# Performance work log

Measured on AMD Instinct MI355X. Metric: run time of the kernel, lower is better.

Reference implementation:

```python
import jax, jax.numpy as jnp
import numpy as np

FLOW_ITERS = 8
DUAL_ITERS = 8
DUAL_STEP = 0.1
DUAL_MOM = 0.9
GRAPH_LAYERS = 2
BIG = 1e9


def _sparsemax(z, mask):
    # sparsemax along last axis; masked entries already hold -BIG, zeroed by mask after.
    V = z.shape[-1]
    zs = jnp.sort(z, axis=-1)[..., ::-1]
    cum = jnp.cumsum(zs, axis=-1)
    k = jnp.arange(1, V + 1, dtype=z.dtype)
    support = zs * k > (cum - 1.0)
    k_sel = jnp.sum(support.astype(jnp.int32), axis=-1, keepdims=True)
    tau = (jnp.take_along_axis(cum, k_sel - 1, axis=-1) - 1.0) / k_sel.astype(z.dtype)
    return jnp.maximum(z - tau, 0.0) * mask


def _min_cost_flow(props, demands):
    # iterative proportional flow routing: push relu(inflow - demand) along predicted proportions
    def body(flow, _):
        inflow = jnp.sum(flow, axis=1)[..., None]      # [B,V,1] inflow to each node
        adjusted = jax.nn.relu(inflow - demands)       # excess to re-route
        return props * adjusted, None                  # row i scaled by its excess
    flow0 = jnp.zeros_like(props)
    flow, _ = jax.lax.scan(body, flow0, None, length=FLOW_ITERS)
    return flow


def _dual_flow(dual_diff, adj):
    # Nesterov-momentum projected gradient on cost(x)=x^2 minus linear dual term, x>=0 on edges
    def body(carry, _):
        flow, acc = carry
        look = flow - DUAL_MOM * acc
        grad = 2.0 * look - dual_diff                  # d/dx x^2 - dual_diff
        acc = DUAL_MOM * acc + DUAL_STEP * grad
        flow = adj * jax.nn.relu(flow - acc)
        return (flow, acc), None
    z = jnp.zeros_like(dual_diff)
    (flow, _), _ = jax.lax.scan(body, (z, z), None, length=DUAL_ITERS)
    return flow


def setup_inputs():
    key = jax.random.key(0)
    ks = jax.random.split(key, 32)
    B, V, F, E, D, K, H = 8, 1200, 8, 16, 64, 2, 4
    node_features = jax.random.normal(ks[0], (B, V, F), dtype=jnp.float32)
    node_embeddings = jax.random.normal(ks[1], (B, V, E), dtype=jnp.float32)
    d = jax.random.normal(ks[2], (B, V, 1), dtype=jnp.float32)
    demands = d - jnp.mean(d, axis=1, keepdims=True)   # balanced supply/demand per graph
    eye = jnp.eye(V, dtype=jnp.float32)
    adj = (jax.random.uniform(ks[3], (B, V, V)) < (16.0 / V)).astype(jnp.float32) * (1.0 - eye)
    hop2 = jnp.clip(adj @ adj, 0.0, 1.0) * (1.0 - eye)
    neighborhoods = jnp.stack([adj, hop2], axis=0)     # [K,B,V,V] k-hop neighborhoods

    def dense(k, fin, fout):
        return (jax.random.normal(k, (fin, fout), dtype=jnp.float32) / np.sqrt(fin)).astype(jnp.float32)

    return dict(
        node_features=node_features, node_embeddings=node_embeddings,
        demands=demands, adj=adj, neighborhoods=neighborhoods,
        enc_w0=dense(ks[4], E + F, D), enc_b0=jnp.zeros((D,), jnp.float32),
        enc_w1=dense(ks[5], D, D), enc_b1=jnp.zeros((D,), jnp.float32),
        agg_w=(jax.random.normal(ks[6], (K, D, D)) / np.sqrt(D)).astype(jnp.float32),
        agg_b=jnp.zeros((K, D), jnp.float32),
        att_w=(jax.random.normal(ks[7], (H, D, D)) / np.sqrt(D)).astype(jnp.float32),
        att_b=jnp.zeros((H, D), jnp.float32),
        att_v=(jax.random.normal(ks[8], (H, D)) / np.sqrt(D)).astype(jnp.float32),
        gru_wu=dense(ks[9], 2 * D, D), gru_bu=jnp.zeros((D,), jnp.float32),
        gru_wr=dense(ks[10], 2 * D, D), gru_br=jnp.zeros((D,), jnp.float32),
        gru_wc=dense(ks[11], 2 * D, D), gru_bc=jnp.zeros((D,), jnp.float32),
        dec_w0=dense(ks[12], D, D), dec_b0=jnp.zeros((D,), jnp.float32),
        dec_w1=dense(ks[13], D, 1), dec_b1=jnp.zeros((1,), jnp.float32),
        dual_w0=dense(ks[14], D, D), dual_b0=jnp.zeros((D,), jnp.float32),
        dual_w1=dense(ks[15], D, 1), dual_b1=jnp.zeros((1,), jnp.float32),
    )


def reference(node_features, node_embeddings, demands, adj, neighborhoods,
              enc_w0, enc_b0, enc_w1, enc_b1, agg_w, agg_b, att_w, att_b, att_v,
              gru_wu, gru_bu, gru_wr, gru_br, gru_wc, gru_bc,
              dec_w0, dec_b0, dec_w1, dec_b1, dual_w0, dual_b0, dual_w1, dual_b1):
    H = att_w.shape[0]
    # node encoder MLP (tanh hidden, tanh final since activate_final=True)
    x = jnp.concatenate([node_embeddings, node_features], axis=-1)
    enc = jnp.tanh(jnp.tanh(x @ enc_w0 + enc_b0) @ enc_w1 + enc_b1)            # [B,V,D]

    deg = jnp.sum(neighborhoods, axis=-1, keepdims=True)
    nb_norm = neighborhoods / jnp.maximum(deg, 1.0)                            # [K,B,V,V]

    for _ in range(GRAPH_LAYERS):
        # per-hop neighborhood aggregation
        msg = jnp.einsum('kbuv,bvd->kbud', nb_norm, enc)
        agg = jnp.tanh(jnp.einsum('kbud,kde->kbue', msg, agg_w) + agg_b[:, None, None, :])
        # multi-head attention over the K hop levels
        proj = jnp.tanh(jnp.einsum('kbvd,hde->hkbve', agg, att_w) + att_b[:, None, None, None, :])
        scores = jnp.einsum('hkbve,he->hkbv', proj, att_v)
        attn = jax.nn.softmax(scores, axis=1)                                  # softmax over hops
        nxt = jnp.einsum('hkbv,kbvd->bvd', attn, agg) / H                      # mean over heads
        # GRU state update
        xs = jnp.concatenate([nxt, enc], axis=-1)
        u = jax.nn.sigmoid(xs @ gru_wu + gru_bu)
        r = jax.nn.sigmoid(xs @ gru_wr + gru_br)
        c = jnp.tanh(jnp.concatenate([nxt, r * enc], axis=-1) @ gru_wc + gru_bc)
        enc = u * enc + (1.0 - u) * c

    # primal: edge weights -> sparsemax -> min-cost-flow
    pred = (enc @ dec_w0 + dec_b0) @ dec_w1 + dec_b1                           # [B,V,1]
    pred_weights = adj * jnp.transpose(pred, (0, 2, 1))                        # [B,V,V]
    weights = -BIG * (1.0 - adj) + pred_weights
    flow_props = _sparsemax(weights, adj)
    flow = _min_cost_flow(flow_props, demands)
    flow_cost = jnp.sum(flow * flow, axis=(1, 2))                              # square cost

    # dual: potentials -> dual-diff -> dual flow solver
    dual = (enc @ dual_w0 + dual_b0) @ dual_w1 + dual_b1                       # [B,V,1]
    dual_diff = adj * (dual - jnp.transpose(dual, (0, 2, 1)))
    dflow = _dual_flow(dual_diff, adj)
    dual_demand = jnp.sum(dual * demands, axis=(1, 2))
    dual_cost = jnp.sum(dflow * dflow - dual_diff * dflow, axis=(1, 2)) - dual_demand

    return flow_cost - dual_cost                                               # duality-gap loss, [B]
```

## Files before the change

### kernel.cpp

```cpp
#include <hip/hip_runtime.h>

#define BB 8
#define VV 1200
#define DD 64
#define KH 2
#define NH 4
#define CAP 64
#define NB2CAP 384
#define NROW (BB*VV)
#define NKROW (KH*BB*VV)

__device__ __forceinline__ float wredsum(float v) {
#pragma unroll
  for (int o = 32; o > 0; o >>= 1) v += __shfl_xor(v, o, 64);
  return v;
}
__device__ __forceinline__ float gredsum32(float v) {
#pragma unroll
  for (int o = 16; o > 0; o >>= 1) v += __shfl_xor(v, o, 64);
  return v;
}

__device__ __forceinline__ float tanh_f(float x) {
  float e = __expf(2.0f * x);
  return 1.0f - 2.0f / (e + 1.0f);
}
__device__ __forceinline__ float sigmoid_f(float x) { return 1.0f / (1.0f + __expf(-x)); }

__device__ __forceinline__ unsigned pack_bf16x2(float a, float b) {
  unsigned ua = __float_as_uint(a), ub = __float_as_uint(b);
  ua = (ua + 0x7fffu + ((ua >> 16) & 1u)) >> 16;
  ub = (ub + 0x7fffu + ((ub >> 16) & 1u)) & 0xffff0000u;
  return ua | ub;
}
__device__ __forceinline__ float bf_lo(unsigned u) { return __uint_as_float(u << 16); }
__device__ __forceinline__ float bf_hi(unsigned u) { return __uint_as_float(u & 0xffff0000u); }

__device__ __forceinline__ size_t nb_base(int row) {
  return (row < NROW) ? (size_t)row * CAP
                      : (size_t)NROW * CAP + (size_t)(row - NROW) * NB2CAP;
}

#define ENC2B (NROW / 64)
#define CSR2B (NKROW / 8)
__global__ void __launch_bounds__(512) k_pre(
    const float* __restrict__ nb, int* __restrict__ nb_cols, int* __restrict__ nb_cnt,
    const float* __restrict__ emb, const float* __restrict__ feat,
    const float* __restrict__ w0, const float* __restrict__ b0,
    const float* __restrict__ w1, const float* __restrict__ b1,
    unsigned* __restrict__ enc0,
    int* __restrict__ col_cnt, float* __restrict__ out, int out_size) {
  __shared__ float Xe[64][25];
  __shared__ float Ht[64][65];
  int bid = blockIdx.x;
  int tid = threadIdx.x;
  if (bid < ENC2B) {
    int tile0 = bid * 64;
    if (tid < 256) {
      int i = tid >> 2, f = tid & 3;
      float4 e4 = *(const float4*)(emb + (size_t)(tile0 + i) * 16 + f * 4);
      Xe[i][f * 4] = e4.x; Xe[i][f * 4 + 1] = e4.y; Xe[i][f * 4 + 2] = e4.z; Xe[i][f * 4 + 3] = e4.w;
    } else if (tid < 384) {
      int t = tid - 256; int i = t >> 1, f = t & 1;
      float4 f4 = *(const float4*)(feat + (size_t)(tile0 + i) * 8 + f * 4);
      Xe[i][16 + f * 4] = f4.x; Xe[i][16 + f * 4 + 1] = f4.y;
      Xe[i][16 + f * 4 + 2] = f4.z; Xe[i][16 + f * 4 + 3] = f4.w;
    }
    __syncthreads();
    int rsub = tid >> 4, cg = tid & 15;
    int c0 = cg * 4, r0 = rsub * 2;
    float a[2][4];
#pragma unroll
    for (int i = 0; i < 2; ++i)
#pragma unroll
      for (int j = 0; j < 4; ++j) a[i][j] = b0[c0 + j];
#pragma unroll
    for (int kk = 0; kk < 24; ++kk) {
      float4 w4 = *(const float4*)(w0 + kk * DD + c0);
      float x0 = Xe[r0][kk], x1 = Xe[r0 + 1][kk];
      a[0][0] = fmaf(x0, w4.x, a[0][0]); a[0][1] = fmaf(x0, w4.y, a[0][1]);
      a[0][2] = fmaf(x0, w4.z, a[0][2]); a[0][3] = fmaf(x0, w4.w, a[0][3]);
      a[1][0] = fmaf(x1, w4.x, a[1][0]); a[1][1] = fmaf(x1, w4.y, a[1][1]);
      a[1][2] = fmaf(x1, w4.z, a[1][2]); a[1][3] = fmaf(x1, w4.w, a[1][3]);
    }
#pragma unroll
    for (int i = 0; i < 2; ++i) {
      Ht[r0 + i][c0] = tanh_f(a[i][0]); Ht[r0 + i][c0 + 1] = tanh_f(a[i][1]);
      Ht[r0 + i][c0 + 2] = tanh_f(a[i][2]); Ht[r0 + i][c0 + 3] = tanh_f(a[i][3]);
    }
    __syncthreads();
    float g[2][4];
#pragma unroll
    for (int i = 0; i < 2; ++i)
#pragma unroll
      for (int j = 0; j < 4; ++j) g[i][j] = b1[c0 + j];
#pragma unroll 8
    for (int kk = 0; kk < DD; ++kk) {
      float4 w4 = *(const float4*)(w1 + kk * DD + c0);
      float x0 = Ht[r0][kk], x1 = Ht[r0 + 1][kk];
      g[0][0] = fmaf(x0, w4.x, g[0][0]); g[0][1] = fmaf(x0, w4.y, g[0][1]);
      g[0][2] = fmaf(x0, w4.z, g[0][2]); g[0][3] = fmaf(x0, w4.w, g[0][3]);
      g[1][0] = fmaf(x1, w4.x, g[1][0]); g[1][1] = fmaf(x1, w4.y, g[1][1]);
      g[1][2] = fmaf(x1, w4.z, g[1][2]); g[1][3] = fmaf(x1, w4.w, g[1][3]);
    }
#pragma unroll
    for (int i = 0; i < 2; ++i) {
      uint2 pk;
      pk.x = pack_bf16x2(tanh_f(g[i][0]), tanh_f(g[i][1]));
      pk.y = pack_bf16x2(tanh_f(g[i][2]), tanh_f(g[i][3]));
      ((uint2*)enc0)[(size_t)(tile0 + r0 + i) * 16 + cg] = pk;
    }
  } else if (bid < ENC2B + CSR2B) {
    int w = tid >> 6, lane = tid & 63;
    int row = (bid - ENC2B) * 8 + w;
    const float4* nb4 = (const float4*)(nb + (size_t)row * VV);
    float4 v[5];
#pragma unroll
    for (int c = 0; c < 4; ++c) v[c] = nb4[c * 64 + lane];
    v[4].x = v[4].y = v[4].z = v[4].w = 0.0f;
    if (lane < 44) v[4] = nb4[256 + lane];
    unsigned long long ltmask = (lane == 0) ? 0ull : ((1ull << lane) - 1ull);
    size_t base = nb_base(row);
    int cap = (row < NROW) ? CAP : NB2CAP;
    int off_base = 0;
#pragma unroll
    for (int c = 0; c < 5; ++c) {
      int nz0 = (v[c].x != 0.0f), nz1 = (v[c].y != 0.0f);
      int nz2 = (v[c].z != 0.0f), nz3 = (v[c].w != 0.0f);
      unsigned long long m0 = __ballot(nz0 != 0);
      unsigned long long m1 = __ballot(nz1 != 0);
      unsigned long long m2 = __ballot(nz2 != 0);
      unsigned long long m3 = __ballot(nz3 != 0);
      int lanepref = __popcll(m0 & ltmask) + __popcll(m1 & ltmask)
                   + __popcll(m2 & ltmask) + __popcll(m3 & ltmask);
      int chunkcnt = __popcll(m0) + __popcll(m1) + __popcll(m2) + __popcll(m3);
      int off = off_base + lanepref;
      int vi = (c * 64 + lane) * 4;
      if (nz0 && off < cap) nb_cols[base + off] = vi;
      off += nz0;
      if (nz1 && off < cap) nb_cols[base + off] = vi + 1;
      off += nz1;
      if (nz2 && off < cap) nb_cols[base + off] = vi + 2;
      off += nz2;
      if (nz3 && off < cap) nb_cols[base + off] = vi + 3;
      off_base += chunkcnt;
    }
    if (lane == 0) nb_cnt[row] = (off_base > cap) ? cap : off_base;
  } else {
    for (int i = tid; i < NROW; i += 512) col_cnt[i] = 0;
    if (tid < out_size) out[tid] = 0.0f;
  }
}

__global__ void __launch_bounds__(256) k_gather(
    const int* __restrict__ nb_cols, const int* __restrict__ nb_cnt,
    const unsigned* __restrict__ encIn, float* __restrict__ msg) {
  int w = threadIdx.x >> 6, lane = threadIdx.x & 63;
  int row = blockIdx.x * 4 + w;
  int k = (row >= NROW) ? 1 : 0;
  int bv = row - k * NROW;
  int b = bv / VV;
  const uint2* encU = (const uint2*)(encIn + (size_t)b * VV * 32);
  const int* cols = nb_cols + nb_base(row);
  int n = nb_cnt[row];
  int sub = lane >> 4, q = lane & 15;
  float ax = 0.0f, ay = 0.0f, az = 0.0f, aw = 0.0f;
  int j = 0;
  int cc0 = 0, cc1 = 0, cc2 = 0, cc3 = 0;
  if (j + 16 <= n) {
    cc0 = cols[j + sub]; cc1 = cols[j + 4 + sub];
    cc2 = cols[j + 8 + sub]; cc3 = cols[j + 12 + sub];
  }
  while (j + 16 <= n) {
    int nj = j + 16;
    int p0 = 0, p1 = 0, p2 = 0, p3 = 0;
    if (nj + 16 <= n) {
      p0 = cols[nj + sub]; p1 = cols[nj + 4 + sub];
      p2 = cols[nj + 8 + sub]; p3 = cols[nj + 12 + sub];
    }
    uint2 u0 = encU[(size_t)cc0 * 16 + q];
    uint2 u1 = encU[(size_t)cc1 * 16 + q];
    uint2 u2 = encU[(size_t)cc2 * 16 + q];
    uint2 u3 = encU[(size_t)cc3 * 16 + q];
    ax += (bf_lo(u0.x) + bf_lo(u1.x)) + (bf_lo(u2.x) + bf_lo(u3.x));
    ay += (bf_hi(u0.x) + bf_hi(u1.x)) + (bf_hi(u2.x) + bf_hi(u3.x));
    az += (bf_lo(u0.y) + bf_lo(u1.y)) + (bf_lo(u2.y) + bf_lo(u3.y));
    aw += (bf_hi(u0.y) + bf_hi(u1.y)) + (bf_hi(u2.y) + bf_hi(u3.y));
    cc0 = p0; cc1 = p1; cc2 = p2; cc3 = p3;
    j = nj;
  }
  for (; j < n; j += 4) {
    int idx = j + sub;
    if (idx < n) {
      uint2 u = encU[(size_t)cols[idx] * 16 + q];
      ax += bf_lo(u.x); ay += bf_hi(u.x); az += bf_lo(u.y); aw += bf_hi(u.y);
    }
  }
#pragma unroll
  for (int o = 16; o < 64; o <<= 1) {
    ax += __shfl_xor(ax, o, 64);
    ay += __shfl_xor(ay, o, 64);
    az += __shfl_xor(az, o, 64);
    aw += __shfl_xor(aw, o, 64);
  }
  if (lane < 16) {
    float inv = 1.0f / fmaxf((float)n, 1.0f);
    float4 r; r.x = ax * inv; r.y = ay * inv; r.z = az * inv; r.w = aw * inv;
    ((float4*)(msg + (size_t)row * DD))[q] = r;
  }
}

__global__ void __launch_bounds__(512) k_mlp(
    const float* __restrict__ msg,
    const float* __restrict__ agg_w, const float* __restrict__ agg_b,
    const float* __restrict__ att_w, const float* __restrict__ att_b,
    const float* __restrict__ att_v,
    float* __restrict__ agg, float* __restrict__ scores) {
  __shared__ float M[64][65];
  __shared__ float G[64][65];
  int tid = threadIdx.x;
  int tile0 = blockIdx.x * 64;
  int k = (tile0 >= NROW) ? 1 : 0;
  int bv0 = tile0 - k * NROW;
  int strip = tid >> 5, cg2 = tid & 31;
  int c0 = cg2 * 2;
  int r0 = strip * 4;
#pragma unroll
  for (int rep = 0; rep < 2; ++rep) {
    int idx = rep * 512 + tid; int i = idx >> 4, d4 = idx & 15;
    float4 m4 = *(const float4*)(msg + (size_t)(tile0 + i) * DD + d4 * 4);
    M[i][d4 * 4] = m4.x; M[i][d4 * 4 + 1] = m4.y; M[i][d4 * 4 + 2] = m4.z; M[i][d4 * 4 + 3] = m4.w;
  }
  __syncthreads();
  const float* W = agg_w + (size_t)k * DD * DD;
  float acc[4][2];
#pragma unroll
  for (int i = 0; i < 4; ++i) {
    acc[i][0] = agg_b[k * DD + c0]; acc[i][1] = agg_b[k * DD + c0 + 1];
  }
#pragma unroll 8
  for (int kk = 0; kk < DD; ++kk) {
    float2 w2 = *(const float2*)(W + kk * DD + c0);
#pragma unroll
    for (int i = 0; i < 4; ++i) {
      float x = M[r0 + i][kk];
      acc[i][0] = fmaf(x, w2.x, acc[i][0]); acc[i][1] = fmaf(x, w2.y, acc[i][1]);
    }
  }
#pragma unroll
  for (int i = 0; i < 4; ++i) {
    float g0 = tanh_f(acc[i][0]), g1 = tanh_f(acc[i][1]);
    G[r0 + i][c0] = g0; G[r0 + i][c0 + 1] = g1;
    *(float2*)(agg + (size_t)(tile0 + r0 + i) * DD + c0) = make_float2(g0, g1);
  }
  __syncthreads();
#pragma unroll
  for (int h = 0; h < NH; ++h) {
    const float* Wh = att_w + (size_t)h * DD * DD;
    float a2[4][2];
#pragma unroll
    for (int i = 0; i < 4; ++i) {
      a2[i][0] = att_b[h * DD + c0]; a2[i][1] = att_b[h * DD + c0 + 1];
    }
#pragma unroll 8
    for (int kk = 0; kk < DD; ++kk) {
      float2 w2 = *(const float2*)(Wh + kk * DD + c0);
#pragma unroll
      for (int i = 0; i < 4; ++i) {
        float x = G[r0 + i][kk];
        a2[i][0] = fmaf(x, w2.x, a2[i][0]); a2[i][1] = fmaf(x, w2.y, a2[i][1]);
      }
    }
    float2 v2 = *(const float2*)(att_v + h * DD + c0);
#pragma unroll
    for (int i = 0; i < 4; ++i) {
      float p = tanh_f(a2[i][0]) * v2.x + tanh_f(a2[i][1]) * v2.y;
      p = gredsum32(p);
      if (cg2 == 0) scores[(size_t)(h * KH + k) * NROW + bv0 + r0 + i] = p;
    }
  }
}

__global__ void __launch_bounds__(128) k_gru(
    const unsigned* __restrict__ encIn, const float* __restrict__ agg,
    const float* __restrict__ scores,
    const float* __restrict__ wu, const float* __restrict__ bu,
    const float* __restrict__ wr, const float* __restrict__ br,
    const float* __restrict__ wc, const float* __restrict__ bc,
    unsigned* __restrict__ encOut,
    int do_decode,
    const float* __restrict__ dw0, const float* __restrict__ db0,
    const float* __restrict__ dw1, const float* __restrict__ db1,
    const float* __restrict__ uw0, const float* __restrict__ ub0,
    const float* __restrict__ uw1, const float* __restrict__ ub1,
    float* __restrict__ pred, float* __restrict__ dualp) {
  __shared__ float X[16][129];
  __shared__ float EO[16][65];
  int tid = threadIdx.x;
  int tile0 = blockIdx.x * 16;
  int strip = tid >> 5, cg2 = tid & 31;
  int c0 = cg2 * 2;
  int r0 = strip * 4;
#pragma unroll
  for (int rep = 0; rep < 2; ++rep) {
    int idx = rep * 128 + tid; int i = idx >> 4, d4 = idx & 15;
    int row = tile0 + i;
    float W0 = 0.0f, W1 = 0.0f;
#pragma unroll
    for (int h = 0; h < NH; ++h) {
      float s0 = scores[(size_t)(h * KH + 0) * NROW + row];
      float s1 = scores[(size_t)(h * KH + 1) * NROW + row];
      float m = fmaxf(s0, s1);
      float e0 = __expf(s0 - m), e1 = __expf(s1 - m);
      float inv = 1.0f / (e0 + e1);
      W0 += e0 * inv; W1 += e1 * inv;
    }
    W0 *= 0.25f; W1 *= 0.25f;
    uint2 eu = ((const uint2*)encIn)[(size_t)row * 16 + d4];
    float4 a0 = *(const float4*)(agg + (size_t)row * DD + d4 * 4);
    float4 a1 = *(const float4*)(agg + (size_t)(NROW + row) * DD + d4 * 4);
    X[i][d4 * 4]     = W0 * a0.x + W1 * a1.x;
    X[i][d4 * 4 + 1] = W0 * a0.y + W1 * a1.y;
    X[i][d4 * 4 + 2] = W0 * a0.z + W1 * a1.z;
    X[i][d4 * 4 + 3] = W0 * a0.w + W1 * a1.w;
    X[i][64 + d4 * 4]     = bf_lo(eu.x);
    X[i][64 + d4 * 4 + 1] = bf_hi(eu.x);
    X[i][64 + d4 * 4 + 2] = bf_lo(eu.y);
    X[i][64 + d4 * 4 + 3] = bf_hi(eu.y);
  }
  __syncthreads();
  float au[4][2], ar[4][2];
#pragma unroll
  for (int i = 0; i < 4; ++i) {
    au[i][0] = bu[c0]; au[i][1] = bu[c0 + 1];
    ar[i][0] = br[c0]; ar[i][1] = br[c0 + 1];
  }
#pragma unroll 8
  for (int kk = 0; kk < 2 * DD; ++kk) {
    float2 u2 = *(const float2*)(wu + kk * DD + c0);
    float2 r2 = *(const float2*)(wr + kk * DD + c0);
#pragma unroll
    for (int i = 0; i < 4; ++i) {
      float x = X[r0 + i][kk];
      au[i][0] = fmaf(x, u2.x, au[i][0]); au[i][1] = fmaf(x, u2.y, au[i][1]);
      ar[i][0] = fmaf(x, r2.x, ar[i][0]); ar[i][1] = fmaf(x, r2.y, ar[i][1]);
    }
  }
  float uu[4][2], encv[4][2];
#pragma unroll
  for (int i = 0; i < 4; ++i) {
    uu[i][0] = sigmoid_f(au[i][0]); uu[i][1] = sigmoid_f(au[i][1]);
    encv[i][0] = X[r0 + i][64 + c0]; encv[i][1] = X[r0 + i][64 + c0 + 1];
  }
  __syncthreads();
#pragma unroll
  for (int i = 0; i < 4; ++i) {
    X[r0 + i][64 + c0]     = encv[i][0] * sigmoid_f(ar[i][0]);
    X[r0 + i][64 + c0 + 1] = encv[i][1] * sigmoid_f(ar[i][1]);
  }
  __syncthreads();
  float ac[4][2];
#pragma unroll
  for (int i = 0; i < 4; ++i) { ac[i][0] = bc[c0]; ac[i][1] = bc[c0 + 1]; }
#pragma unroll 8
  for (int kk = 0; kk < 2 * DD; ++kk) {
    float2 c2 = *(const float2*)(wc + kk * DD + c0);
#pragma unroll
    for (int i = 0; i < 4; ++i) {
      float x = X[r0 + i][kk];
      ac[i][0] = fmaf(x, c2.x, ac[i][0]); ac[i][1] = fmaf(x, c2.y, ac[i][1]);
    }
  }
#pragma unroll
  for (int i = 0; i < 4; ++i) {
    float e0 = uu[i][0] * encv[i][0] + (1.0f - uu[i][0]) * tanh_f(ac[i][0]);
    float e1 = uu[i][1] * encv[i][1] + (1.0f - uu[i][1]) * tanh_f(ac[i][1]);
    ((unsigned*)encOut)[(size_t)(tile0 + r0 + i) * 32 + cg2] = pack_bf16x2(e0, e1);
    EO[r0 + i][c0] = e0; EO[r0 + i][c0 + 1] = e1;
  }
  if (do_decode) {
    __syncthreads();
    float hd[4][2], hq[4][2];
#pragma unroll
    for (int i = 0; i < 4; ++i) {
      hd[i][0] = db0[c0]; hd[i][1] = db0[c0 + 1];
      hq[i][0] = ub0[c0]; hq[i][1] = ub0[c0 + 1];
    }
#pragma unroll 8
    for (int kk = 0; kk < DD; ++kk) {
      float2 d2 = *(const float2*)(dw0 + kk * DD + c0);
      float2 q2 = *(const float2*)(uw0 + kk * DD + c0);
#pragma unroll
      for (int i = 0; i < 4; ++i) {
        float x = EO[r0 + i][kk];
        hd[i][0] = fmaf(x, d2.x, hd[i][0]); hd[i][1] = fmaf(x, d2.y, hd[i][1]);
        hq[i][0] = fmaf(x, q2.x, hq[i][0]); hq[i][1] = fmaf(x, q2.y, hq[i][1]);
      }
    }
    float2 dv = *(const float2*)(dw1 + c0);
    float2 qv = *(const float2*)(uw1 + c0);
#pragma unroll
    for (int i = 0; i < 4; ++i) {
      float p = hd[i][0] * dv.x + hd[i][1] * dv.y;
      float q = hq[i][0] * qv.x + hq[i][1] * qv.y;
      p = gredsum32(p);
      q = gredsum32(q);
      if (cg2 == 0) {
        pred[tile0 + r0 + i] = p + db1[0];
        dualp[tile0 + r0 + i] = q + ub1[0];
      }
    }
  }
}

__global__ void __launch_bounds__(256) k_primal_dual(
    const int* __restrict__ nb_cols, const int* __restrict__ nb_cnt,
    const float* __restrict__ pred, const float* __restrict__ dualp,
    const float* __restrict__ dem,
    float* __restrict__ rowsum,
    int* __restrict__ col_cnt, int* __restrict__ col_rows, float* __restrict__ col_vals,
    float* __restrict__ out) {
  __shared__ float bacc[BB];
  if (threadIdx.x < BB) bacc[threadIdx.x] = 0.0f;
  __syncthreads();
  int w = threadIdx.x >> 6, lane = threadIdx.x & 63;
  int row = blockIdx.x * 4 + w;
  int b = row / VV;
  int n = nb_cnt[row];
  int c = (lane < n) ? nb_cols[(size_t)row * CAP + lane] : 0;
  const float* predB = pred + (size_t)b * VV;
  const float* dualB = dualp + (size_t)b * VV;
  float z = (lane < n) ? predB[c] : -1e30f;
  float tau = 0.0f;
  if (n > 0) {
    bool in = (lane < n);
    for (int it = 0; it < 64; ++it) {
      float s = wredsum(in ? z : 0.0f);
      int cnt = (int)__popcll(__ballot(in));
      tau = (s - 1.0f) / (float)cnt;
      bool nin = (z > tau);
      if (__ballot(nin) == __ballot(in)) break;
      in = nin;
    }
  }
  float pv = (lane < n) ? fmaxf(z - tau, 0.0f) : 0.0f;
  float s2 = wredsum(pv * pv);
  if (lane == 0) rowsum[row] = s2;
  if (pv > 0.0f) {
    int g = b * VV + c;
    int j = atomicAdd(&col_cnt[g], 1);
    if (j < CAP) {
      col_rows[(size_t)g * CAP + j] = row - b * VV;
      col_vals[(size_t)g * CAP + j] = pv;
    }
  }
  float du = dualp[row];
  float es = 0.0f;
  if (lane < n) {
    float dd = du - dualB[c];
    float f = 0.0f, acm = 0.0f;
#pragma unroll
    for (int t = 0; t < 8; ++t) {
      float look = f - 0.9f * acm;
      float grad = 2.0f * look - dd;
      acm = 0.9f * acm + 0.1f * grad;
      f = fmaxf(f - acm, 0.0f);
    }
    es = f * f - dd * f;
  }
  float contrib = -es;
  if (lane == 0) contrib += du * dem[row];
  float ws_ = wredsum(contrib);
  if (lane == 0) atomicAdd(&bacc[b], ws_);
  __syncthreads();
  if (threadIdx.x < BB) {
    float t = bacc[threadIdx.x];
    if (t != 0.0f) atomicAdd(&out[threadIdx.x], t);
  }
}

__global__ void __launch_bounds__(1024) k_flow(
    const int* __restrict__ col_cnt, const int* __restrict__ col_rows,
    const float* __restrict__ col_vals, const float* __restrict__ dem,
    const float* __restrict__ rowsum, float* __restrict__ out) {
  __shared__ float aS[VV];
  __shared__ float red[16];
  int b = blockIdx.x;
  int tid = threadIdx.x;
  const float* demB = dem + (size_t)b * VV;
  for (int v = tid; v < VV; v += 1024) aS[v] = fmaxf(-demB[v], 0.0f);
  __syncthreads();
  for (int t = 0; t < 7; ++t) {
    float nv0 = 0.0f, nv1 = 0.0f;
    {
      int v = tid;
      if (v < VV) {
        int g = b * VV + v;
        int n = col_cnt[g]; if (n > CAP) n = CAP;
        const int* cr = col_rows + (size_t)g * CAP;
        const float* cv = col_vals + (size_t)g * CAP;
        float acc = 0.0f;
        for (int j = 0; j < n; ++j) acc += cv[j] * aS[cr[j]];
        nv0 = fmaxf(acc - demB[v], 0.0f);
      }
      v = tid + 1024;
      if (v < VV) {
        int g = b * VV + v;
        int n = col_cnt[g]; if (n > CAP) n = CAP;
        const int* cr = col_rows + (size_t)g * CAP;
        const float* cv = col_vals + (size_t)g * CAP;
        float acc = 0.0f;
        for (int j = 0; j < n; ++j) acc += cv[j] * aS[cr[j]];
        nv1 = fmaxf(acc - demB[v], 0.0f);
      }
    }
    __syncthreads();
    if (tid < VV) aS[tid] = nv0;
    if (tid + 1024 < VV) aS[tid + 1024] = nv1;
    __syncthreads();
  }
  float fc = 0.0f;
  for (int v = tid; v < VV; v += 1024) { float a = aS[v]; fc += a * a * rowsum[b * VV + v]; }
  fc = wredsum(fc);
  int wid = tid >> 6, lane = tid & 63;
  if (lane == 0) red[wid] = fc;
  __syncthreads();
  if (tid == 0) {
    float s = 0.0f;
#pragma unroll
    for (int i = 0; i < 16; ++i) s += red[i];
    atomicAdd(&out[b], s);
  }
}

extern "C" void kernel_launch(void* const* d_in, const int* in_sizes, int n_in,
                              void* d_out, int out_size, void* d_ws, size_t ws_size,
                              hipStream_t stream) {
  const float* feat   = (const float*)d_in[0];
  const float* emb    = (const float*)d_in[1];
  const float* dem    = (const float*)d_in[2];
  const float* nb     = (const float*)d_in[4];
  const float* enc_w0 = (const float*)d_in[5];
  const float* enc_b0 = (const float*)d_in[6];
  const float* enc_w1 = (const float*)d_in[7];
  const float* enc_b1 = (const float*)d_in[8];
  const float* agg_w  = (const float*)d_in[9];
  const float* agg_b  = (const float*)d_in[10];
  const float* att_w  = (const float*)d_in[11];
  const float* att_b  = (const float*)d_in[12];
  const float* att_v  = (const float*)d_in[13];
  const float* gru_wu = (const float*)d_in[14];
  const float* gru_bu = (const float*)d_in[15];
  const float* gru_wr = (const float*)d_in[16];
  const float* gru_br = (const float*)d_in[17];
  const float* gru_wc = (const float*)d_in[18];
  const float* gru_bc = (const float*)d_in[19];
  const float* dec_w0 = (const float*)d_in[20];
  const float* dec_b0 = (const float*)d_in[21];
  const float* dec_w1 = (const float*)d_in[22];
  const float* dec_b1 = (const float*)d_in[23];
  const float* dual_w0= (const float*)d_in[24];
  const float* dual_b0= (const float*)d_in[25];
  const float* dual_w1= (const float*)d_in[26];
  const float* dual_b1= (const float*)d_in[27];
  float* out = (float*)d_out;

  unsigned* enc0 = (unsigned*)d_ws;
  unsigned* enc1 = enc0 + (size_t)NROW * 32;
  float* msg      = (float*)(enc1 + (size_t)NROW * 32);
  float* aggbuf   = msg + (size_t)NKROW * DD;
  float* scores   = aggbuf + (size_t)NKROW * DD;
  float* pred     = scores + (size_t)NH * KH * NROW;
  float* dualp    = pred + NROW;
  float* rowsum   = dualp + NROW;
  float* col_vals = rowsum + NROW;
  int* col_cnt  = (int*)(col_vals + (size_t)NROW * CAP);
  int* nb_cnt   = col_cnt + NROW;
  int* col_rows = nb_cnt + NKROW;
  int* nb_cols  = col_rows + (size_t)NROW * CAP;

  (void)in_sizes; (void)n_in; (void)ws_size;

  k_pre<<<ENC2B + CSR2B + 1, 512, 0, stream>>>(
      nb, nb_cols, nb_cnt, emb, feat, enc_w0, enc_b0, enc_w1, enc_b1, enc0,
      col_cnt, out, out_size);

  const unsigned* encIn = enc0;
  unsigned* encOut = enc1;
  for (int l = 0; l < 2; ++l) {
    k_gather<<<NKROW / 4, 256, 0, stream>>>(nb_cols, nb_cnt, encIn, msg);
    k_mlp<<<NKROW / 64, 512, 0, stream>>>(msg, agg_w, agg_b, att_w, att_b, att_v,
                                          aggbuf, scores);
    k_gru<<<NROW / 16, 128, 0, stream>>>(encIn, aggbuf, scores,
                                         gru_wu, gru_bu, gru_wr, gru_br, gru_wc, gru_bc,
                                         encOut,
                                         (l == 1) ? 1 : 0,
                                         dec_w0, dec_b0, dec_w1, dec_b1,
                                         dual_w0, dual_b0, dual_w1, dual_b1, pred, dualp);
    const unsigned* t = encIn; encIn = encOut; encOut = (unsigned*)t;
  }

  k_primal_dual<<<NROW / 4, 256, 0, stream>>>(nb_cols, nb_cnt, pred, dualp, dem,
                                              rowsum, col_cnt, col_rows, col_vals, out);
  k_flow<<<BB, 1024, 0, stream>>>(col_cnt, col_rows, col_vals, dem, rowsum, out);
}
```

Measured before the change: 506.2 us.

## Store encodings in fp32 and stage CSR column lists in shared memory

Node encodings move from packed bf16 to plain fp32 across the pre, gather and GRU kernels, which removes the pack and unpack arithmetic but doubles the bytes read per neighbour in the gather. In addition, the CSR build writes each row's column indices into a per-wave shared buffer first, then copies them to global memory in a coalesced loop instead of scattering them. The extra 12 KB of shared memory in k_pre may lower occupancy, and the heavier gather traffic could outweigh the saved conversion work.

```diff
diff --git a/kernel.cpp b/kernel.cpp
--- a/kernel.cpp
+++ b/kernel.cpp
@@ -27,15 +27,6 @@
 }
 __device__ __forceinline__ float sigmoid_f(float x) { return 1.0f / (1.0f + __expf(-x)); }
 
-__device__ __forceinline__ unsigned pack_bf16x2(float a, float b) {
-  unsigned ua = __float_as_uint(a), ub = __float_as_uint(b);
-  ua = (ua + 0x7fffu + ((ua >> 16) & 1u)) >> 16;
-  ub = (ub + 0x7fffu + ((ub >> 16) & 1u)) & 0xffff0000u;
-  return ua | ub;
-}
-__device__ __forceinline__ float bf_lo(unsigned u) { return __uint_as_float(u << 16); }
-__device__ __forceinline__ float bf_hi(unsigned u) { return __uint_as_float(u & 0xffff0000u); }
-
 __device__ __forceinline__ size_t nb_base(int row) {
   return (row < NROW) ? (size_t)row * CAP
                       : (size_t)NROW * CAP + (size_t)(row - NROW) * NB2CAP;
@@ -48,10 +39,11 @@
     const float* __restrict__ emb, const float* __restrict__ feat,
     const float* __restrict__ w0, const float* __restrict__ b0,
     const float* __restrict__ w1, const float* __restrict__ b1,
-    unsigned* __restrict__ enc0,
+    float* __restrict__ enc0,
     int* __restrict__ col_cnt, float* __restrict__ out, int out_size) {
   __shared__ float Xe[64][25];
   __shared__ float Ht[64][65];
+  __shared__ int colS[8][NB2CAP];
   int bid = blockIdx.x;
   int tid = threadIdx.x;
   if (bid < ENC2B) {
@@ -105,10 +97,10 @@
     }
 #pragma unroll
     for (int i = 0; i < 2; ++i) {
-      uint2 pk;
-      pk.x = pack_bf16x2(tanh_f(g[i][0]), tanh_f(g[i][1]));
-      pk.y = pack_bf16x2(tanh_f(g[i][2]), tanh_f(g[i][3]));
-      ((uint2*)enc0)[(size_t)(tile0 + r0 + i) * 16 + cg] = pk;
+      float4 o;
+      o.x = tanh_f(g[i][0]); o.y = tanh_f(g[i][1]);
+      o.z = tanh_f(g[i][2]); o.w = tanh_f(g[i][3]);
+      *(float4*)(enc0 + (size_t)(tile0 + r0 + i) * DD + c0) = o;
     }
   } else if (bid < ENC2B + CSR2B) {
     int w = tid >> 6, lane = tid & 63;
@@ -136,16 +128,18 @@
       int chunkcnt = __popcll(m0) + __popcll(m1) + __popcll(m2) + __popcll(m3);
       int off = off_base + lanepref;
       int vi = (c * 64 + lane) * 4;
-      if (nz0 && off < cap) nb_cols[base + off] = vi;
+      if (nz0 && off < cap) colS[w][off] = vi;
       off += nz0;
-      if (nz1 && off < cap) nb_cols[base + off] = vi + 1;
+      if (nz1 && off < cap) colS[w][off] = vi + 1;
       off += nz1;
-      if (nz2 && off < cap) nb_cols[base + off] = vi + 2;
+      if (nz2 && off < cap) colS[w][off] = vi + 2;
       off += nz2;
-      if (nz3 && off < cap) nb_cols[base + off] = vi + 3;
+      if (nz3 && off < cap) colS[w][off] = vi + 3;
       off_base += chunkcnt;
     }
-    if (lane == 0) nb_cnt[row] = (off_base > cap) ? cap : off_base;
+    int ncp = (off_base > cap) ? cap : off_base;
+    if (lane == 0) nb_cnt[row] = ncp;
+    for (int j = lane; j < ncp; j += 64) nb_cols[base + j] = colS[w][j];
   } else {
     for (int i = tid; i < NROW; i += 512) col_cnt[i] = 0;
     if (tid < out_size) out[tid] = 0.0f;
@@ -154,13 +148,13 @@
 
 __global__ void __launch_bounds__(256) k_gather(
     const int* __restrict__ nb_cols, const int* __restrict__ nb_cnt,
-    const unsigned* __restrict__ encIn, float* __restrict__ msg) {
+    const float* __restrict__ encIn, float* __restrict__ msg) {
   int w = threadIdx.x >> 6, lane = threadIdx.x & 63;
   int row = blockIdx.x * 4 + w;
   int k = (row >= NROW) ? 1 : 0;
   int bv = row - k * NROW;
   int b = bv / VV;
-  const uint2* encU = (const uint2*)(encIn + (size_t)b * VV * 32);
+  const float4* encF = (const float4*)(encIn + (size_t)b * VV * DD);
   const int* cols = nb_cols + nb_base(row);
   int n = nb_cnt[row];
   int sub = lane >> 4, q = lane & 15;
@@ -178,22 +172,22 @@
       p0 = cols[nj + sub]; p1 = cols[nj + 4 + sub];
       p2 = cols[nj + 8 + sub]; p3 = cols[nj + 12 + sub];
     }
-    uint2 u0 = encU[(size_t)cc0 * 16 + q];
-    uint2 u1 = encU[(size_t)cc1 * 16 + q];
-    uint2 u2 = encU[(size_t)cc2 * 16 + q];
-    uint2 u3 = encU[(size_t)cc3 * 16 + q];
-    ax += (bf_lo(u0.x) + bf_lo(u1.x)) + (bf_lo(u2.x) + bf_lo(u3.x));
-    ay += (bf_hi(u0.x) + bf_hi(u1.x)) + (bf_hi(u2.x) + bf_hi(u3.x));
-    az += (bf_lo(u0.y) + bf_lo(u1.y)) + (bf_lo(u2.y) + bf_lo(u3.y));
-    aw += (bf_hi(u0.y) + bf_hi(u1.y)) + (bf_hi(u2.y) + bf_hi(u3.y));
+    float4 u0 = encF[(size_t)cc0 * 16 + q];
+    float4 u1 = encF[(size_t)cc1 * 16 + q];
+    float4 u2 = encF[(size_t)cc2 * 16 + q];
+    float4 u3 = encF[(size_t)cc3 * 16 + q];
+    ax += (u0.x + u1.x) + (u2.x + u3.x);
+    ay += (u0.y + u1.y) + (u2.y + u3.y);
+    az += (u0.z + u1.z) + (u2.z + u3.z);
+    aw += (u0.w + u1.w) + (u2.w + u3.w);
     cc0 = p0; cc1 = p1; cc2 = p2; cc3 = p3;
     j = nj;
   }
   for (; j < n; j += 4) {
     int idx = j + sub;
     if (idx < n) {
-      uint2 u = encU[(size_t)cols[idx] * 16 + q];
-      ax += bf_lo(u.x); ay += bf_hi(u.x); az += bf_lo(u.y); aw += bf_hi(u.y);
+      float4 u = encF[(size_t)cols[idx] * 16 + q];
+      ax += u.x; ay += u.y; az += u.z; aw += u.w;
     }
   }
 #pragma unroll
@@ -282,12 +276,12 @@
 }
 
 __global__ void __launch_bounds__(128) k_gru(
-    const unsigned* __restrict__ encIn, const float* __restrict__ agg,
+    const float* __restrict__ encIn, const float* __restrict__ agg,
     const float* __restrict__ scores,
     const float* __restrict__ wu, const float* __restrict__ bu,
     const float* __restrict__ wr, const float* __restrict__ br,
     const float* __restrict__ wc, const float* __restrict__ bc,
-    unsigned* __restrict__ encOut,
+    float* __restrict__ encOut,
     int do_decode,
     const float* __restrict__ dw0, const float* __restrict__ db0,
     const float* __restrict__ dw1, const float* __restrict__ db1,
@@ -316,17 +310,17 @@
       W0 += e0 * inv; W1 += e1 * inv;
     }
     W0 *= 0.25f; W1 *= 0.25f;
-    uint2 eu = ((const uint2*)encIn)[(size_t)row * 16 + d4];
+    float4 ef = *(const float4*)(encIn + (size_t)row * DD + d4 * 4);
     float4 a0 = *(const float4*)(agg + (size_t)row * DD + d4 * 4);
     float4 a1 = *(const float4*)(agg + (size_t)(NROW + row) * DD + d4 * 4);
     X[i][d4 * 4]     = W0 * a0.x + W1 * a1.x;
     X[i][d4 * 4 + 1] = W0 * a0.y + W1 * a1.y;
     X[i][d4 * 4 + 2] = W0 * a0.z + W1 * a1.z;
     X[i][d4 * 4 + 3] = W0 * a0.w + W1 * a1.w;
-    X[i][64 + d4 * 4]     = bf_lo(eu.x);
-    X[i][64 + d4 * 4 + 1] = bf_hi(eu.x);
-    X[i][64 + d4 * 4 + 2] = bf_lo(eu.y);
-    X[i][64 + d4 * 4 + 3] = bf_hi(eu.y);
+    X[i][64 + d4 * 4]     = ef.x;
+    X[i][64 + d4 * 4 + 1] = ef.y;
+    X[i][64 + d4 * 4 + 2] = ef.z;
+    X[i][64 + d4 * 4 + 3] = ef.w;
   }
   __syncthreads();
   float au[4][2], ar[4][2];
@@ -375,7 +369,7 @@
   for (int i = 0; i < 4; ++i) {
     float e0 = uu[i][0] * encv[i][0] + (1.0f - uu[i][0]) * tanh_f(ac[i][0]);
     float e1 = uu[i][1] * encv[i][1] + (1.0f - uu[i][1]) * tanh_f(ac[i][1]);
-    ((unsigned*)encOut)[(size_t)(tile0 + r0 + i) * 32 + cg2] = pack_bf16x2(e0, e1);
+    *(float2*)(encOut + (size_t)(tile0 + r0 + i) * DD + c0) = make_float2(e0, e1);
     EO[r0 + i][c0] = e0; EO[r0 + i][c0 + 1] = e1;
   }
   if (do_decode) {
@@ -565,9 +559,9 @@
   const float* dual_b1= (const float*)d_in[27];
   float* out = (float*)d_out;
 
-  unsigned* enc0 = (unsigned*)d_ws;
-  unsigned* enc1 = enc0 + (size_t)NROW * 32;
-  float* msg      = (float*)(enc1 + (size_t)NROW * 32);
+  float* enc0 = (float*)d_ws;
+  float* enc1 = enc0 + (size_t)NROW * DD;
+  float* msg      = enc1 + (size_t)NROW * DD;
   float* aggbuf   = msg + (size_t)NKROW * DD;
   float* scores   = aggbuf + (size_t)NKROW * DD;
   float* pred     = scores + (size_t)NH * KH * NROW;
@@ -585,8 +579,8 @@
       nb, nb_cols, nb_cnt, emb, feat, enc_w0, enc_b0, enc_w1, enc_b1, enc0,
       col_cnt, out, out_size);
 
-  const unsigned* encIn = enc0;
-  unsigned* encOut = enc1;
+  const float* encIn = enc0;
+  float* encOut = enc1;
   for (int l = 0; l < 2; ++l) {
     k_gather<<<NKROW / 4, 256, 0, stream>>>(nb_cols, nb_cnt, encIn, msg);
     k_mlp<<<NKROW / 64, 512, 0, stream>>>(msg, agg_w, agg_b, att_w, att_b, att_v,
@@ -597,7 +591,7 @@
                                          (l == 1) ? 1 : 0,
                                          dec_w0, dec_b0, dec_w1, dec_b1,
                                          dual_w0, dual_b0, dual_w1, dual_b1, pred, dualp);
-    const unsigned* t = encIn; encIn = encOut; encOut = (unsigned*)t;
+    const float* t = encIn; encIn = encOut; encOut = (float*)t;
   }
 
   k_primal_dual<<<NROW / 4, 256, 0, stream>>>(nb_cols, nb_cnt, pred, dualp, dem,
```

New measurement: 513.4 us. No clear change (+1.4%).
